# Kernel tuning notes

Hardware: AMD Instinct MI355X
Metric: run time of the kernel (lower is better)

The kernel has to match this reference:

```python
import jax, jax.numpy as jnp
import numpy as np
from jax import lax

# --- constants derived from init args ---
TAU = 0.1
CNSTS = (1.0, 10.0)
EPSILON = CNSTS[0] / TAU          # 10.0
LAMBDAA = CNSTS[0] * CNSTS[1] / TAU  # 100.0
ALPHA = 0.5
SIGMA = 2.0
ITER_NUM = 5
IN_CHANNELS = 3
M = max(4 * int(2 * SIGMA) + 1, 5)  # 17


def gauss_kernel():
    # 2D normalized Gaussian, shape [C, 1, M, M] for depthwise conv (OIHW with groups=C)
    xx = jnp.arange(M, dtype=jnp.float32) - (M - 1.0) / 2.0
    d2 = xx[:, None] ** 2 + xx[None, :] ** 2
    w = jnp.exp(-d2 / (2.0 * SIGMA ** 2))
    w = w / w.sum()
    return jnp.broadcast_to(w[None, None], (IN_CHANNELS, 1, M, M))


def depthwise_conv(x, w):
    # x: [B, C, H, W], w: [C, 1, M, M]; SAME padding (M odd, pad = M//2)
    return lax.conv_general_dilated(
        x, w, window_strides=(1, 1), padding='SAME',
        dimension_numbers=('NCHW', 'OIHW', 'NCHW'),
        feature_group_count=IN_CHANNELS)


def setup_inputs() -> dict:
    key = jax.random.key(0)
    k1, k2 = jax.random.split(key)
    x = jax.random.uniform(k1, (8, 3, 512, 512), dtype=jnp.float32)
    c = jax.random.normal(k2, (8, 3, 512, 512), dtype=jnp.float32)
    return {'x': x, 'c': c}


def reference(x, c):
    w = gauss_kernel()
    b = jax.nn.sigmoid(10.0 * c)          # getb(c)
    lam_b = LAMBDAA * b
    u = jax.nn.sigmoid(-(lam_b * depthwise_conv(1.0 - 2.0 * x, w)) / EPSILON)
    for _ in range(max(abs(ITER_NUM), 1)):
        uu = (u - x) / TAU + lam_b * depthwise_conv(1.0 - 2.0 * u, w)
        uu = jax.nn.sigmoid(-uu / EPSILON)
        u = (1.0 - ALPHA) * u + ALPHA * uu
    return u
```

## Files before the change

kernel.cpp:

```cpp
#include <hip/hip_runtime.h>
#include <hip/hip_fp16.h>
#include <math.h>


#define TILE 64
#define RAD  8
#define HW   512
#define NIMG 24
#define NPIX ((size_t)HW * HW * NIMG)

__device__ __constant__ const float GWc[17] = {
    6.6916e-05f, 4.3635e-04f, 2.2159612e-03f, 8.7643070e-03f,
    2.6995958e-02f, 6.4759932e-02f, 1.2098751e-01f, 1.7603572e-01f,
    1.9947466e-01f,
    1.7603572e-01f, 1.2098751e-01f, 6.4759932e-02f, 2.6995958e-02f,
    8.7643070e-03f, 2.2159612e-03f, 4.3635e-04f, 6.6916e-05f
};

struct alignas(8)  H4 { __half2 a, b; };
struct alignas(16) H8 { __half2 a, b, c, d; };

__device__ __forceinline__ float inv1pexp(float z) {
    return __builtin_amdgcn_rcpf(1.0f + __expf(z));
}

template<int MODE>
__global__ __launch_bounds__(256, 6) void sig_step(
    const float* __restrict__ xg, const float* __restrict__ cgl,
    const __half* __restrict__ uin, __half2* __restrict__ xl,
    void* __restrict__ uout)
{
    __shared__ __half sTmp[80 * TILE];

    const int t    = threadIdx.x;
    const int img  = blockIdx.z;
    const int row0 = blockIdx.y * TILE;
    const int col0 = blockIdx.x * TILE;
    const size_t ibase = (size_t)img * HW * HW;

#pragma unroll
    for (int i = 0; i < 3; ++i) {
        int q = t + i * 256;
        if (q < 640) {
            int r  = q >> 3;
            int ci = q & 7;
            int gr = row0 + r - RAD;
            float w[24];
#pragma unroll
            for (int j = 0; j < 24; ++j) w[j] = 0.f;
            if (gr >= 0 && gr < HW) {
                int gc0 = col0 + ci * 8 - RAD;
                if constexpr (MODE == 0) {
                    const float* xb = xg + ibase + (size_t)gr * HW;
#pragma unroll
                    for (int j = 0; j < 6; ++j) {
                        int s = gc0 + 4 * j;
                        if (s >= 0 && s <= HW - 4) {
                            float4 v = *reinterpret_cast<const float4*>(&xb[s]);
                            w[4*j+0] = 1.f - 2.f * v.x;
                            w[4*j+1] = 1.f - 2.f * v.y;
                            w[4*j+2] = 1.f - 2.f * v.z;
                            w[4*j+3] = 1.f - 2.f * v.w;
                        }
                    }
                } else {
                    const __half* ub = uin + ibase + (size_t)gr * HW;
#pragma unroll
                    for (int j = 0; j < 3; ++j) {
                        int s = gc0 + 8 * j;
                        if (s >= 0 && s <= HW - 8) {
                            H8 v = *reinterpret_cast<const H8*>(&ub[s]);
                            float2 f0 = __half22float2(v.a);
                            float2 f1 = __half22float2(v.b);
                            float2 f2 = __half22float2(v.c);
                            float2 f3 = __half22float2(v.d);
                            w[8*j+0] = 1.f - 2.f * f0.x;
                            w[8*j+1] = 1.f - 2.f * f0.y;
                            w[8*j+2] = 1.f - 2.f * f1.x;
                            w[8*j+3] = 1.f - 2.f * f1.y;
                            w[8*j+4] = 1.f - 2.f * f2.x;
                            w[8*j+5] = 1.f - 2.f * f2.y;
                            w[8*j+6] = 1.f - 2.f * f3.x;
                            w[8*j+7] = 1.f - 2.f * f3.y;
                        }
                    }
                }
            }
            float a[8];
#pragma unroll
            for (int j = 0; j < 8; ++j) {
                float acc = 0.f;
#pragma unroll
                for (int k = 0; k < 17; ++k) acc += GWc[k] * w[j + k];
                a[j] = acc;
            }
            H8 o;
            o.a = __floats2half2_rn(a[0], a[1]);
            o.b = __floats2half2_rn(a[2], a[3]);
            o.c = __floats2half2_rn(a[4], a[5]);
            o.d = __floats2half2_rn(a[6], a[7]);
            *reinterpret_cast<H8*>(&sTmp[r * TILE + ci * 8]) = o;
        }
    }
    __syncthreads();

    const int cc = t & 63;
    const int rg = t >> 6;
    const size_t pbase = ibase + (size_t)(row0 + rg * 16) * HW + (col0 + cc);

    float win[32];
#pragma unroll
    for (int j = 0; j < 32; ++j)
        win[j] = __half2float(sTmp[(rg * 16 + j) * TILE + cc]);

#pragma unroll
    for (int m = 0; m < 16; ++m) {
        float acc = 0.f;
#pragma unroll
        for (int k = 0; k < 17; ++k) acc += GWc[k] * win[m + k];

        size_t gidx = pbase + (size_t)m * HW;
        if constexpr (MODE == 0) {
            float xv  = xg[gidx];
            float lam = 100.f * inv1pexp(-10.f * cgl[gidx]);
            xl[gidx] = __floats2half2_rn(xv, lam);
            ((__half*)uout)[gidx] = __float2half(inv1pexp(lam * acc * 0.1f));
        } else {
            float2 p = __half22float2(xl[gidx]);
            float uprev = __half2float(uin[gidx]);
            float tt = (uprev - p.x) * 10.f + p.y * acc;
            float uu = inv1pexp(tt * 0.1f);
            float res = 0.5f * uprev + 0.5f * uu;
            if constexpr (MODE == 2) ((float*)uout)[gidx] = res;
            else                     ((__half*)uout)[gidx] = __float2half(res);
        }
    }
}

extern "C" void kernel_launch(void* const* d_in, const int* in_sizes, int n_in,
                              void* d_out, int out_size, void* d_ws, size_t ws_size,
                              hipStream_t stream) {
    const float* x = (const float*)d_in[0];
    const float* c = (const float*)d_in[1];

    __half* u0 = (__half*)d_ws;
    __half* u1 = u0 + NPIX;
    __half2* xl = (ws_size >= NPIX * 8)
        ? (__half2*)((char*)d_ws + NPIX * 4)
        : (__half2*)d_out;

    dim3 grid(HW / TILE, HW / TILE, NIMG);
    dim3 block(256);
    sig_step<0><<<grid, block, 0, stream>>>(x, c, nullptr, xl, u0);
    sig_step<1><<<grid, block, 0, stream>>>(x, c, u0, xl, u1);
    sig_step<1><<<grid, block, 0, stream>>>(x, c, u1, xl, u0);
    sig_step<1><<<grid, block, 0, stream>>>(x, c, u0, xl, u1);
    sig_step<1><<<grid, block, 0, stream>>>(x, c, u1, xl, u0);
    sig_step<2><<<grid, block, 0, stream>>>(x, c, u0, xl, d_out);
}
```

Measured before the change: 116.6 us.

## Fuse pairs of iterations per kernel using halo recompute in shared memory

Each kernel now runs two solver steps per tile. It loads a 16-pixel halo, computes the intermediate u over an 80x80 region in shared memory, then applies the second blur and update, so six launches become three. The precomputed packed x/lambda buffer is dropped and lambda is recomputed from c on each pass. This trades extra halo recompute, more shared memory and lower occupancy (launch bounds 6 to 5) for halved global round trips of u and fewer launches.

```diff
diff --git a/kernel.cpp b/kernel.cpp
--- a/kernel.cpp
+++ b/kernel.cpp
@@ -4,7 +4,6 @@
 
 
 #define TILE 64
-#define RAD  8
 #define HW   512
 #define NIMG 24
 #define NPIX ((size_t)HW * HW * NIMG)
@@ -17,20 +16,28 @@
     8.7643070e-03f, 2.2159612e-03f, 4.3635e-04f, 6.6916e-05f
 };
 
-struct alignas(8)  H4 { __half2 a, b; };
 struct alignas(16) H8 { __half2 a, b, c, d; };
 
 __device__ __forceinline__ float inv1pexp(float z) {
     return __builtin_amdgcn_rcpf(1.0f + __expf(z));
 }
 
+__device__ __forceinline__ H8 pack8(const float* a) {
+    H8 o;
+    o.a = __floats2half2_rn(a[0], a[1]);
+    o.b = __floats2half2_rn(a[2], a[3]);
+    o.c = __floats2half2_rn(a[4], a[5]);
+    o.d = __floats2half2_rn(a[6], a[7]);
+    return o;
+}
+
 template<int MODE>
-__global__ __launch_bounds__(256, 6) void sig_step(
+__global__ __launch_bounds__(256, 5) void sig_pair(
     const float* __restrict__ xg, const float* __restrict__ cgl,
-    const __half* __restrict__ uin, __half2* __restrict__ xl,
-    void* __restrict__ uout)
+    const __half* __restrict__ uin, void* __restrict__ uout)
 {
-    __shared__ __half sTmp[80 * TILE];
+    __shared__ __half sA[96 * 80];
+    __shared__ __half sU[80 * 80];
 
     const int t    = threadIdx.x;
     const int img  = blockIdx.z;
@@ -39,23 +46,23 @@
     const size_t ibase = (size_t)img * HW * HW;
 
 #pragma unroll
-    for (int i = 0; i < 3; ++i) {
+    for (int i = 0; i < 4; ++i) {
         int q = t + i * 256;
-        if (q < 640) {
-            int r  = q >> 3;
-            int ci = q & 7;
-            int gr = row0 + r - RAD;
+        if (q < 960) {
+            int r  = q / 10;
+            int ci = q - r * 10;
+            int gr  = row0 + r - 16;
+            int gc0 = col0 + ci * 8 - 16;
             float w[24];
 #pragma unroll
             for (int j = 0; j < 24; ++j) w[j] = 0.f;
             if (gr >= 0 && gr < HW) {
-                int gc0 = col0 + ci * 8 - RAD;
                 if constexpr (MODE == 0) {
                     const float* xb = xg + ibase + (size_t)gr * HW;
 #pragma unroll
                     for (int j = 0; j < 6; ++j) {
                         int s = gc0 + 4 * j;
-                        if (s >= 0 && s <= HW - 4) {
+                        if (s >= 0 && s < HW) {
                             float4 v = *reinterpret_cast<const float4*>(&xb[s]);
                             w[4*j+0] = 1.f - 2.f * v.x;
                             w[4*j+1] = 1.f - 2.f * v.y;
@@ -68,7 +75,7 @@
 #pragma unroll
                     for (int j = 0; j < 3; ++j) {
                         int s = gc0 + 8 * j;
-                        if (s >= 0 && s <= HW - 8) {
+                        if (s >= 0 && s < HW) {
                             H8 v = *reinterpret_cast<const H8*>(&ub[s]);
                             float2 f0 = __half22float2(v.a);
                             float2 f1 = __half22float2(v.b);
@@ -94,24 +101,113 @@
                 for (int k = 0; k < 17; ++k) acc += GWc[k] * w[j + k];
                 a[j] = acc;
             }
-            H8 o;
-            o.a = __floats2half2_rn(a[0], a[1]);
-            o.b = __floats2half2_rn(a[2], a[3]);
-            o.c = __floats2half2_rn(a[4], a[5]);
-            o.d = __floats2half2_rn(a[6], a[7]);
-            *reinterpret_cast<H8*>(&sTmp[r * TILE + ci * 8]) = o;
+            *reinterpret_cast<H8*>(&sA[r * 80 + ci * 8]) = pack8(a);
+        }
+    }
+    __syncthreads();
+
+#pragma unroll
+    for (int i = 0; i < 4; ++i) {
+        int q = t + i * 256;
+        if (q < 800) {
+            int r  = q / 10;
+            int ci = q - r * 10;
+            float a0=0.f,a1=0.f,a2=0.f,a3=0.f,a4=0.f,a5=0.f,a6=0.f,a7=0.f;
+#pragma unroll
+            for (int k = 0; k < 17; ++k) {
+                H8 v = *reinterpret_cast<const H8*>(&sA[(r + k) * 80 + ci * 8]);
+                float g = GWc[k];
+                float2 f0 = __half22float2(v.a);
+                float2 f1 = __half22float2(v.b);
+                float2 f2 = __half22float2(v.c);
+                float2 f3 = __half22float2(v.d);
+                a0 += g * f0.x; a1 += g * f0.y; a2 += g * f1.x; a3 += g * f1.y;
+                a4 += g * f2.x; a5 += g * f2.y; a6 += g * f3.x; a7 += g * f3.y;
+            }
+            float acc[8] = { a0,a1,a2,a3,a4,a5,a6,a7 };
+            int gr  = row0 + r - 8;
+            int gc0 = col0 + ci * 8 - 8;
+            float res[8];
+            if (gr >= 0 && gr < HW && gc0 >= 0 && gc0 < HW) {
+                size_t gb = ibase + (size_t)gr * HW + gc0;
+                float4 c0 = *reinterpret_cast<const float4*>(&cgl[gb]);
+                float4 c1 = *reinterpret_cast<const float4*>(&cgl[gb + 4]);
+                float cv[8] = { c0.x,c0.y,c0.z,c0.w, c1.x,c1.y,c1.z,c1.w };
+                if constexpr (MODE == 0) {
+#pragma unroll
+                    for (int j = 0; j < 8; ++j) {
+                        float lam = 100.f * inv1pexp(-10.f * cv[j]);
+                        res[j] = inv1pexp(lam * acc[j] * 0.1f);
+                    }
+                } else {
+                    H8 u8 = *reinterpret_cast<const H8*>(&uin[gb]);
+                    float2 u0 = __half22float2(u8.a), u1 = __half22float2(u8.b);
+                    float2 u2 = __half22float2(u8.c), u3 = __half22float2(u8.d);
+                    float up[8] = { u0.x,u0.y,u1.x,u1.y,u2.x,u2.y,u3.x,u3.y };
+                    float4 x0 = *reinterpret_cast<const float4*>(&xg[gb]);
+                    float4 x1 = *reinterpret_cast<const float4*>(&xg[gb + 4]);
+                    float xv[8] = { x0.x,x0.y,x0.z,x0.w, x1.x,x1.y,x1.z,x1.w };
+#pragma unroll
+                    for (int j = 0; j < 8; ++j) {
+                        float lam = 100.f * inv1pexp(-10.f * cv[j]);
+                        float tt  = (up[j] - xv[j]) * 10.f + lam * acc[j];
+                        float uu  = inv1pexp(tt * 0.1f);
+                        res[j] = 0.5f * (up[j] + uu);
+                    }
+                }
+            } else {
+#pragma unroll
+                for (int j = 0; j < 8; ++j) res[j] = 0.5f;
+            }
+            *reinterpret_cast<H8*>(&sU[r * 80 + ci * 8]) = pack8(res);
+        }
+    }
+    __syncthreads();
+
+    __half* sB = sA;
+#pragma unroll
+    for (int i = 0; i < 3; ++i) {
+        int q = t + i * 256;
+        if (q < 640) {
+            int r  = q >> 3;
+            int ci = q & 7;
+            float w[24];
+#pragma unroll
+            for (int jj = 0; jj < 3; ++jj) {
+                H8 v = *reinterpret_cast<const H8*>(&sU[r * 80 + ci * 8 + jj * 8]);
+                float2 f0 = __half22float2(v.a);
+                float2 f1 = __half22float2(v.b);
+                float2 f2 = __half22float2(v.c);
+                float2 f3 = __half22float2(v.d);
+                w[8*jj+0] = 1.f - 2.f * f0.x;
+                w[8*jj+1] = 1.f - 2.f * f0.y;
+                w[8*jj+2] = 1.f - 2.f * f1.x;
+                w[8*jj+3] = 1.f - 2.f * f1.y;
+                w[8*jj+4] = 1.f - 2.f * f2.x;
+                w[8*jj+5] = 1.f - 2.f * f2.y;
+                w[8*jj+6] = 1.f - 2.f * f3.x;
+                w[8*jj+7] = 1.f - 2.f * f3.y;
+            }
+            float a[8];
+#pragma unroll
+            for (int j = 0; j < 8; ++j) {
+                float acc = 0.f;
+#pragma unroll
+                for (int k = 0; k < 17; ++k) acc += GWc[k] * w[j + k];
+                a[j] = acc;
+            }
+            *reinterpret_cast<H8*>(&sB[r * 64 + ci * 8]) = pack8(a);
         }
     }
     __syncthreads();
 
     const int cc = t & 63;
     const int rg = t >> 6;
-    const size_t pbase = ibase + (size_t)(row0 + rg * 16) * HW + (col0 + cc);
-
+    const __half* sBr = sA;
     float win[32];
 #pragma unroll
     for (int j = 0; j < 32; ++j)
-        win[j] = __half2float(sTmp[(rg * 16 + j) * TILE + cc]);
+        win[j] = __half2float(sBr[(rg * 16 + j) * 64 + cc]);
 
 #pragma unroll
     for (int m = 0; m < 16; ++m) {
@@ -119,21 +215,15 @@
 #pragma unroll
         for (int k = 0; k < 17; ++k) acc += GWc[k] * win[m + k];
 
-        size_t gidx = pbase + (size_t)m * HW;
-        if constexpr (MODE == 0) {
-            float xv  = xg[gidx];
-            float lam = 100.f * inv1pexp(-10.f * cgl[gidx]);
-            xl[gidx] = __floats2half2_rn(xv, lam);
-            ((__half*)uout)[gidx] = __float2half(inv1pexp(lam * acc * 0.1f));
-        } else {
-            float2 p = __half22float2(xl[gidx]);
-            float uprev = __half2float(uin[gidx]);
-            float tt = (uprev - p.x) * 10.f + p.y * acc;
-            float uu = inv1pexp(tt * 0.1f);
-            float res = 0.5f * uprev + 0.5f * uu;
-            if constexpr (MODE == 2) ((float*)uout)[gidx] = res;
-            else                     ((__half*)uout)[gidx] = __float2half(res);
-        }
+        size_t gidx = ibase + (size_t)(row0 + rg * 16 + m) * HW + (col0 + cc);
+        float uprev = __half2float(sU[(rg * 16 + m + 8) * 80 + (cc + 8)]);
+        float lam = 100.f * inv1pexp(-10.f * cgl[gidx]);
+        float xv  = xg[gidx];
+        float tt  = (uprev - xv) * 10.f + lam * acc;
+        float uu  = inv1pexp(tt * 0.1f);
+        float res = 0.5f * (uprev + uu);
+        if constexpr (MODE == 2) ((float*)uout)[gidx] = res;
+        else                     ((__half*)uout)[gidx] = __float2half(res);
     }
 }
 
@@ -143,18 +233,12 @@
     const float* x = (const float*)d_in[0];
     const float* c = (const float*)d_in[1];
 
-    __half* u0 = (__half*)d_ws;
-    __half* u1 = u0 + NPIX;
-    __half2* xl = (ws_size >= NPIX * 8)
-        ? (__half2*)((char*)d_ws + NPIX * 4)
-        : (__half2*)d_out;
+    __half* u2 = (__half*)d_ws;
+    __half* u4 = u2 + NPIX;
 
     dim3 grid(HW / TILE, HW / TILE, NIMG);
     dim3 block(256);
-    sig_step<0><<<grid, block, 0, stream>>>(x, c, nullptr, xl, u0);
-    sig_step<1><<<grid, block, 0, stream>>>(x, c, u0, xl, u1);
-    sig_step<1><<<grid, block, 0, stream>>>(x, c, u1, xl, u0);
-    sig_step<1><<<grid, block, 0, stream>>>(x, c, u0, xl, u1);
-    sig_step<1><<<grid, block, 0, stream>>>(x, c, u1, xl, u0);
-    sig_step<2><<<grid, block, 0, stream>>>(x, c, u0, xl, d_out);
-}
+    sig_pair<0><<<grid, block, 0, stream>>>(x, c, nullptr, u2);
+    sig_pair<1><<<grid, block, 0, stream>>>(x, c, u2, u4);
+    sig_pair<2><<<grid, block, 0, stream>>>(x, c, u4, d_out);
+}
```

Result: slower. 139.6 us (+19.7%).

## Shrink row tile to 32 and apply affine 1-2u after convolution

Applied to the files above, without the earlier changes.

Changes tiles from 64x64 to 32x64 rows, shrinking shared memory and register windows and raising launch bounds to 8 blocks per SM. The 1-2x transform is moved after the separable Gaussian blur, using padding value 0.5 so the algebra stays exact under zero padding. The goal is higher occupancy and fewer per-element ops in the horizontal pass. The cost is a larger halo overhead, since 48 rows are loaded per 32 output rows instead of 80 per 64.

```diff
diff --git a/kernel.cpp b/kernel.cpp
--- a/kernel.cpp
+++ b/kernel.cpp
@@ -3,7 +3,9 @@
 #include <math.h>
 
 
-#define TILE 64
+#define TR   32
+#define TC   64
+#define HR   48
 #define RAD  8
 #define HW   512
 #define NIMG 24
@@ -17,7 +19,6 @@
     8.7643070e-03f, 2.2159612e-03f, 4.3635e-04f, 6.6916e-05f
 };
 
-struct alignas(8)  H4 { __half2 a, b; };
 struct alignas(16) H8 { __half2 a, b, c, d; };
 
 __device__ __forceinline__ float inv1pexp(float z) {
@@ -25,29 +26,29 @@
 }
 
 template<int MODE>
-__global__ __launch_bounds__(256, 6) void sig_step(
+__global__ __launch_bounds__(256, 8) void sig_step(
     const float* __restrict__ xg, const float* __restrict__ cgl,
     const __half* __restrict__ uin, __half2* __restrict__ xl,
     void* __restrict__ uout)
 {
-    __shared__ __half sTmp[80 * TILE];
+    __shared__ __half sTmp[HR * TC];
 
     const int t    = threadIdx.x;
     const int img  = blockIdx.z;
-    const int row0 = blockIdx.y * TILE;
-    const int col0 = blockIdx.x * TILE;
+    const int row0 = blockIdx.y * TR;
+    const int col0 = blockIdx.x * TC;
     const size_t ibase = (size_t)img * HW * HW;
 
 #pragma unroll
-    for (int i = 0; i < 3; ++i) {
+    for (int i = 0; i < 2; ++i) {
         int q = t + i * 256;
-        if (q < 640) {
+        if (q < HR * 8) {
             int r  = q >> 3;
             int ci = q & 7;
             int gr = row0 + r - RAD;
             float w[24];
 #pragma unroll
-            for (int j = 0; j < 24; ++j) w[j] = 0.f;
+            for (int j = 0; j < 24; ++j) w[j] = 0.5f;
             if (gr >= 0 && gr < HW) {
                 int gc0 = col0 + ci * 8 - RAD;
                 if constexpr (MODE == 0) {
@@ -55,12 +56,10 @@
 #pragma unroll
                     for (int j = 0; j < 6; ++j) {
                         int s = gc0 + 4 * j;
-                        if (s >= 0 && s <= HW - 4) {
+                        if (s >= 0 && s < HW) {
                             float4 v = *reinterpret_cast<const float4*>(&xb[s]);
-                            w[4*j+0] = 1.f - 2.f * v.x;
-                            w[4*j+1] = 1.f - 2.f * v.y;
-                            w[4*j+2] = 1.f - 2.f * v.z;
-                            w[4*j+3] = 1.f - 2.f * v.w;
+                            w[4*j+0] = v.x; w[4*j+1] = v.y;
+                            w[4*j+2] = v.z; w[4*j+3] = v.w;
                         }
                     }
                 } else {
@@ -68,20 +67,16 @@
 #pragma unroll
                     for (int j = 0; j < 3; ++j) {
                         int s = gc0 + 8 * j;
-                        if (s >= 0 && s <= HW - 8) {
+                        if (s >= 0 && s < HW) {
                             H8 v = *reinterpret_cast<const H8*>(&ub[s]);
                             float2 f0 = __half22float2(v.a);
                             float2 f1 = __half22float2(v.b);
                             float2 f2 = __half22float2(v.c);
                             float2 f3 = __half22float2(v.d);
-                            w[8*j+0] = 1.f - 2.f * f0.x;
-                            w[8*j+1] = 1.f - 2.f * f0.y;
-                            w[8*j+2] = 1.f - 2.f * f1.x;
-                            w[8*j+3] = 1.f - 2.f * f1.y;
-                            w[8*j+4] = 1.f - 2.f * f2.x;
-                            w[8*j+5] = 1.f - 2.f * f2.y;
-                            w[8*j+6] = 1.f - 2.f * f3.x;
-                            w[8*j+7] = 1.f - 2.f * f3.y;
+                            w[8*j+0] = f0.x; w[8*j+1] = f0.y;
+                            w[8*j+2] = f1.x; w[8*j+3] = f1.y;
+                            w[8*j+4] = f2.x; w[8*j+5] = f2.y;
+                            w[8*j+6] = f3.x; w[8*j+7] = f3.y;
                         }
                     }
                 }
@@ -99,38 +94,39 @@
             o.b = __floats2half2_rn(a[2], a[3]);
             o.c = __floats2half2_rn(a[4], a[5]);
             o.d = __floats2half2_rn(a[6], a[7]);
-            *reinterpret_cast<H8*>(&sTmp[r * TILE + ci * 8]) = o;
+            *reinterpret_cast<H8*>(&sTmp[r * TC + ci * 8]) = o;
         }
     }
     __syncthreads();
 
     const int cc = t & 63;
     const int rg = t >> 6;
-    const size_t pbase = ibase + (size_t)(row0 + rg * 16) * HW + (col0 + cc);
+    const size_t pbase = ibase + (size_t)(row0 + rg * 8) * HW + (col0 + cc);
 
-    float win[32];
+    float win[24];
 #pragma unroll
-    for (int j = 0; j < 32; ++j)
-        win[j] = __half2float(sTmp[(rg * 16 + j) * TILE + cc]);
+    for (int j = 0; j < 24; ++j)
+        win[j] = __half2float(sTmp[(rg * 8 + j) * TC + cc]);
 
 #pragma unroll
-    for (int m = 0; m < 16; ++m) {
-        float acc = 0.f;
+    for (int m = 0; m < 8; ++m) {
+        float v = 0.f;
 #pragma unroll
-        for (int k = 0; k < 17; ++k) acc += GWc[k] * win[m + k];
+        for (int k = 0; k < 17; ++k) v += GWc[k] * win[m + k];
+        float f = 1.f - 2.f * v;
 
         size_t gidx = pbase + (size_t)m * HW;
         if constexpr (MODE == 0) {
             float xv  = xg[gidx];
             float lam = 100.f * inv1pexp(-10.f * cgl[gidx]);
             xl[gidx] = __floats2half2_rn(xv, lam);
-            ((__half*)uout)[gidx] = __float2half(inv1pexp(lam * acc * 0.1f));
+            ((__half*)uout)[gidx] = __float2half(inv1pexp(lam * f * 0.1f));
         } else {
             float2 p = __half22float2(xl[gidx]);
             float uprev = __half2float(uin[gidx]);
-            float tt = (uprev - p.x) * 10.f + p.y * acc;
+            float tt = (uprev - p.x) * 10.f + p.y * f;
             float uu = inv1pexp(tt * 0.1f);
-            float res = 0.5f * uprev + 0.5f * uu;
+            float res = 0.5f * (uprev + uu);
             if constexpr (MODE == 2) ((float*)uout)[gidx] = res;
             else                     ((__half*)uout)[gidx] = __float2half(res);
         }
@@ -149,7 +145,7 @@
         ? (__half2*)((char*)d_ws + NPIX * 4)
         : (__half2*)d_out;
 
-    dim3 grid(HW / TILE, HW / TILE, NIMG);
+    dim3 grid(HW / TC, HW / TR, NIMG);
     dim3 block(256);
     sig_step<0><<<grid, block, 0, stream>>>(x, c, nullptr, xl, u0);
     sig_step<1><<<grid, block, 0, stream>>>(x, c, u0, xl, u1);
```

Result: no change. 116.4 us (-0.1%).
